# Performance work log

Measured on AMD Instinct MI355X. Metric: run time of the kernel, lower is better.

Reference implementation:

```python
import jax, jax.numpy as jnp
import numpy as np

B, D_IN, NQ, H = 65536, 385, 64, 16  # batch, input dim, num questions, head width
DIMS = [385, 512, 256, 192]


def setup_inputs() -> dict:
    key = jax.random.key(0)
    ks = jax.random.split(key, 12)
    s = 0.02
    inp = {
        "x": jax.random.normal(ks[0], (B, D_IN), jnp.float32),
        "W1": jax.random.normal(ks[1], (DIMS[0], DIMS[1]), jnp.float32) * s,
        "b1": jnp.zeros((DIMS[1],), jnp.float32),
        "W2": jax.random.normal(ks[2], (DIMS[1], DIMS[2]), jnp.float32) * s,
        "b2": jnp.zeros((DIMS[2],), jnp.float32),
        "W3": jax.random.normal(ks[3], (DIMS[2], DIMS[3]), jnp.float32) * s,
        "b3": jnp.zeros((DIMS[3],), jnp.float32),
        # all true/false heads stacked: layout [qid, correct, H] flattened on last axis
        "Wh": jax.random.normal(ks[4], (DIMS[3], NQ * 2 * H), jnp.float32) * s,
        "bh": jnp.zeros((NQ * 2 * H,), jnp.float32),
        "question_ids": jax.random.randint(ks[5], (B,), 0, NQ, jnp.int32),
        "is_correct": jax.random.randint(ks[6], (B,), 0, 2, jnp.int32),
    }
    return inp


def reference(x, W1, b1, W2, b2, W3, b3, Wh, bh, question_ids, is_correct):
    # shared trunk (dropout is identity at eval); activation = relu
    h = jax.nn.relu(x @ W1 + b1)          # [B, 512]
    h = jax.nn.relu(h @ W2 + b2)          # [B, 256]
    h = jax.nn.relu(h @ W3 + b3)          # [B, 192] shared features
    # compute all heads densely, then gather the per-row head slice —
    # equivalent to routing each row to its (question_id, is_correct) Linear head
    logits_all = h @ Wh + bh              # [B, NQ*2*H]
    base = (question_ids * 2 + is_correct) * H        # [B]
    idx = base[:, None] + jnp.arange(H)[None, :]      # [B, H]
    return jnp.take_along_axis(logits_all, idx, axis=1)  # [B, H]
```

## Files before the change

### kernel.cpp

```cpp
#include <hip/hip_runtime.h>
#include <hip/hip_bf16.h>

#define THREADS 1024
#define ROWS 64

typedef __attribute__((ext_vector_type(4))) float f32x4;
typedef __attribute__((ext_vector_type(8))) short s16x8;

__device__ __forceinline__ unsigned short bfbits(float f) {
  __bf16 h = (__bf16)f;
  return __builtin_bit_cast(unsigned short, h);
}
__device__ __forceinline__ float bf2f(unsigned short h) {
  unsigned u = ((unsigned)h) << 16;
  return __builtin_bit_cast(float, u);
}

__global__ void prep_kernel(const float* __restrict__ W1, const float* __restrict__ W2,
                            const float* __restrict__ W3, const float* __restrict__ Wh,
                            unsigned short* __restrict__ w1f, unsigned short* __restrict__ w2f,
                            unsigned short* __restrict__ w3f, unsigned short* __restrict__ whT) {
  int u = blockIdx.x * blockDim.x + threadIdx.x;
  const int U1 = 24576, U2 = 16384, U3 = 6144, U4 = 49152;
  if (u < U1) {
    int lane = u & 63, r = (u >> 6) & 31, c = u >> 11;
    int f  = r * 16 + (lane & 15);
    int kb = c * 32 + ((lane >> 4) << 3);
    s16x8 v;
    #pragma unroll
    for (int j = 0; j < 8; ++j) v[j] = (short)bfbits(W1[(kb + j) * 512 + f]);
    *(s16x8*)(w1f + (u << 3)) = v;
    return;
  }
  u -= U1;
  if (u < U2) {
    int lane = u & 63, r = (u >> 6) & 15, c = u >> 10;
    int f  = r * 16 + (lane & 15);
    int kb = c * 32 + ((lane >> 4) << 3);
    s16x8 v;
    #pragma unroll
    for (int j = 0; j < 8; ++j) v[j] = (short)bfbits(W2[(kb + j) * 256 + f]);
    *(s16x8*)(w2f + (u << 3)) = v;
    return;
  }
  u -= U2;
  if (u < U3) {
    int lane = u & 63, t = u >> 6;
    int c = t / 12, r = t - c * 12;
    int f  = r * 16 + (lane & 15);
    int kb = c * 32 + ((lane >> 4) << 3);
    s16x8 v;
    #pragma unroll
    for (int j = 0; j < 8; ++j) v[j] = (short)bfbits(W3[(kb + j) * 192 + f]);
    *(s16x8*)(w3f + (u << 3)) = v;
    return;
  }
  u -= U3;
  if (u < U4) {
    int j = u & 15, v2 = u >> 4;
    int fo = v2 % 24, head = v2 / 24;
    s16x8 v;
    #pragma unroll
    for (int i = 0; i < 8; ++i) v[i] = (short)bfbits(Wh[(fo * 8 + i) * 2048 + head * 16 + j]);
    *(s16x8*)(whT + u * 8) = v;
  }
}

#define MFMA(a, b, c) __builtin_amdgcn_mfma_f32_16x16x32_bf16((a), (b), (c), 0, 0, 0)
#define SWZ(lane) (((lane) * 16) ^ ((((lane) >> 4) & 3) << 5))

__global__ __launch_bounds__(THREADS, 4)
void fused_mlp(const float* __restrict__ x,
               const float* __restrict__ b1,
               const float* __restrict__ b2,
               const float* __restrict__ b3,
               const float* __restrict__ bh,
               const float* __restrict__ W1,
               const int* __restrict__ qid,
               const int* __restrict__ corr,
               const unsigned short* __restrict__ w1f,
               const unsigned short* __restrict__ w2f,
               const unsigned short* __restrict__ w3f,
               const unsigned short* __restrict__ whT,
               float* __restrict__ out) {
  __shared__ __align__(16) unsigned char lds[120832];
  unsigned char* xall = lds;
  unsigned char* h1f  = lds + 49152;
  unsigned char* h2f  = lds;
  float* h3p          = (float*)(lds + 49152);
  float* b1s  = (float*)(lds + 114688);
  float* b2s  = (float*)(lds + 116736);
  float* b3s  = (float*)(lds + 117760);
  float* w1l  = (float*)(lds + 118528);
  float* x384 = (float*)(lds + 120576);

  const int tid  = threadIdx.x;
  const int lane = tid & 63;
  const int w    = tid >> 6;
  const int b0   = blockIdx.x * ROWS;
  const int l15  = lane & 15;
  const int lh   = lane >> 4;

  const int s_kh = tid & 3;
  const int s_sr = (tid >> 2) & 63;
  const int s_cl = tid >> 8;
  const int s_off = ((s_sr >> 4) << 10) + SWZ((s_sr & 15) + (s_kh << 4));
  const float* s_x = x + (size_t)(b0 + s_sr) * 385 + (s_kh << 3);

  f32x4 lo, hi;
  auto sload = [&](int p) {
    int c = (p << 2) + s_cl;
    lo = *(const f32x4*)(s_x + c * 32);
    hi = *(const f32x4*)(s_x + c * 32 + 4);
  };
  auto swrite = [&](int p) {
    int c = (p << 2) + s_cl;
    s16x8 v;
    v[0] = (short)bfbits(lo[0]); v[1] = (short)bfbits(lo[1]);
    v[2] = (short)bfbits(lo[2]); v[3] = (short)bfbits(lo[3]);
    v[4] = (short)bfbits(hi[0]); v[5] = (short)bfbits(hi[1]);
    v[6] = (short)bfbits(hi[2]); v[7] = (short)bfbits(hi[3]);
    *(s16x8*)(xall + (c << 12) + s_off) = v;
  };

  sload(0);
  if (tid < 512)                    { b1s[tid] = b1[tid]; w1l[tid] = W1[384 * 512 + tid]; }
  else if (tid < 768)               { b2s[tid - 512] = b2[tid - 512]; }
  else if (tid < 960)               { b3s[tid - 768] = b3[tid - 768]; }
  else                              { x384[tid - 960] = x[(size_t)(b0 + tid - 960) * 385 + 384]; }
  swrite(0);
  __syncthreads();

  f32x4 acc1[2][4];
  #pragma unroll
  for (int a = 0; a < 2; ++a)
    #pragma unroll
    for (int bt = 0; bt < 4; ++bt) acc1[a][bt] = (f32x4)0.0f;

  const int swz_l = SWZ(lane);

#define G1_CHUNKS(C0, C1)                                                              \
  _Pragma("unroll")                                                                    \
  for (int c = C0; c < C1; ++c) {                                                      \
    s16x8 a0 = *(const s16x8*)(w1f + (((c * 32 + w * 2 + 0) * 64 + lane) << 3));       \
    s16x8 a1 = *(const s16x8*)(w1f + (((c * 32 + w * 2 + 1) * 64 + lane) << 3));       \
    _Pragma("unroll")                                                                  \
    for (int bt = 0; bt < 4; ++bt) {                                                   \
      s16x8 bfr = *(const s16x8*)(xall + (c << 12) + (bt << 10) + swz_l);              \
      acc1[0][bt] = MFMA(a0, bfr, acc1[0][bt]);                                        \
      acc1[1][bt] = MFMA(a1, bfr, acc1[1][bt]);                                        \
    }                                                                                  \
  }

  sload(1);
  G1_CHUNKS(0, 4)
  swrite(1);
  __syncthreads();

  sload(2);
  G1_CHUNKS(4, 8)
  swrite(2);
  __syncthreads();

  G1_CHUNKS(8, 12)

  #pragma unroll
  for (int a = 0; a < 2; ++a) {
    int ft = w * 2 + a;
    int fb = (ft << 4) + (lh << 2);
    f32x4 bv = *(const f32x4*)(b1s + fb);
    f32x4 wv = *(const f32x4*)(w1l + fb);
    int kh = ((a << 1) + (lh >> 1)) & 3;
    int so = SWZ(l15 + (kh << 4)) + ((lh & 1) << 3);
    #pragma unroll
    for (int bt = 0; bt < 4; ++bt) {
      float xv = x384[(bt << 4) + l15];
      float v0 = fmaxf(acc1[a][bt][0] + bv[0] + wv[0] * xv, 0.f);
      float v1 = fmaxf(acc1[a][bt][1] + bv[1] + wv[1] * xv, 0.f);
      float v2 = fmaxf(acc1[a][bt][2] + bv[2] + wv[2] * xv, 0.f);
      float v3 = fmaxf(acc1[a][bt][3] + bv[3] + wv[3] * xv, 0.f);
      unsigned plo = (unsigned)bfbits(v0) | ((unsigned)bfbits(v1) << 16);
      unsigned phi = (unsigned)bfbits(v2) | ((unsigned)bfbits(v3) << 16);
      unsigned long long pk = (unsigned long long)plo | ((unsigned long long)phi << 32);
      *(unsigned long long*)(h1f + (((w << 2) + bt) << 10) + so) = pk;
    }
  }
  __syncthreads();

  f32x4 acc2[4];
  #pragma unroll
  for (int bt = 0; bt < 4; ++bt) acc2[bt] = (f32x4)0.0f;

  #pragma unroll
  for (int c = 0; c < 16; ++c) {
    s16x8 a2 = *(const s16x8*)(w2f + (((c * 16 + w) * 64 + lane) << 3));
    #pragma unroll
    for (int bt = 0; bt < 4; ++bt) {
      s16x8 bfr = *(const s16x8*)(h1f + ((c << 12) + (bt << 10)) + swz_l);
      acc2[bt] = MFMA(a2, bfr, acc2[bt]);
    }
  }

  {
    int fb = (w << 4) + (lh << 2);
    f32x4 bv = *(const f32x4*)(b2s + fb);
    int kh = (((w & 1) << 1) + (lh >> 1)) & 3;
    int so = SWZ(l15 + (kh << 4)) + ((lh & 1) << 3);
    #pragma unroll
    for (int bt = 0; bt < 4; ++bt) {
      float v0 = fmaxf(acc2[bt][0] + bv[0], 0.f);
      float v1 = fmaxf(acc2[bt][1] + bv[1], 0.f);
      float v2 = fmaxf(acc2[bt][2] + bv[2], 0.f);
      float v3 = fmaxf(acc2[bt][3] + bv[3], 0.f);
      unsigned plo = (unsigned)bfbits(v0) | ((unsigned)bfbits(v1) << 16);
      unsigned phi = (unsigned)bfbits(v2) | ((unsigned)bfbits(v3) << 16);
      unsigned long long pk = (unsigned long long)plo | ((unsigned long long)phi << 32);
      *(unsigned long long*)(h2f + ((((w >> 1) << 2) + bt) << 10) + so) = pk;
    }
  }
  __syncthreads();

  if (w < 12) {
    f32x4 acc3[4];
    #pragma unroll
    for (int bt = 0; bt < 4; ++bt) acc3[bt] = (f32x4)0.0f;

    #pragma unroll
    for (int c = 0; c < 8; ++c) {
      s16x8 a3 = *(const s16x8*)(w3f + (((c * 12 + w) * 64 + lane) << 3));
      #pragma unroll
      for (int bt = 0; bt < 4; ++bt) {
        s16x8 bfr = *(const s16x8*)(h2f + ((c << 12) + (bt << 10)) + swz_l);
        acc3[bt] = MFMA(a3, bfr, acc3[bt]);
      }
    }

    int fb = (w << 4) + (lh << 2);
    f32x4 bv = *(const f32x4*)(b3s + fb);
    #pragma unroll
    for (int bt = 0; bt < 4; ++bt) {
      int bb = (bt << 4) + l15;
      f32x4 vv;
      vv[0] = fmaxf(acc3[bt][0] + bv[0], 0.f);
      vv[1] = fmaxf(acc3[bt][1] + bv[1], 0.f);
      vv[2] = fmaxf(acc3[bt][2] + bv[2], 0.f);
      vv[3] = fmaxf(acc3[bt][3] + bv[3], 0.f);
      *(f32x4*)(h3p + bb * 204 + fb) = vv;
    }
  }
  __syncthreads();

  {
    int bb = tid >> 4, j = tid & 15;
    int gb = b0 + bb;
    int head = qid[gb] * 2 + corr[gb];
    const unsigned short* wp = whT + ((head * 24) * 16 + j) * 8;
    const float* hp = h3p + bb * 204;
    float acc = bh[(head << 4) + j];
    #pragma unroll 6
    for (int fo = 0; fo < 24; ++fo) {
      s16x8 wv = *(const s16x8*)(wp + fo * 128);
      f32x4 h0 = *(const f32x4*)(hp + fo * 8);
      f32x4 h1v = *(const f32x4*)(hp + fo * 8 + 4);
      acc += bf2f((unsigned short)wv[0]) * h0[0] + bf2f((unsigned short)wv[1]) * h0[1]
           + bf2f((unsigned short)wv[2]) * h0[2] + bf2f((unsigned short)wv[3]) * h0[3]
           + bf2f((unsigned short)wv[4]) * h1v[0] + bf2f((unsigned short)wv[5]) * h1v[1]
           + bf2f((unsigned short)wv[6]) * h1v[2] + bf2f((unsigned short)wv[7]) * h1v[3];
    }
    out[(size_t)gb * 16 + j] = acc;
  }
}

extern "C" void kernel_launch(void* const* d_in, const int* in_sizes, int n_in,
                              void* d_out, int out_size, void* d_ws, size_t ws_size,
                              hipStream_t stream) {
  (void)in_sizes; (void)n_in; (void)out_size; (void)ws_size;
  const float* x  = (const float*)d_in[0];
  const float* W1 = (const float*)d_in[1];
  const float* b1 = (const float*)d_in[2];
  const float* W2 = (const float*)d_in[3];
  const float* b2 = (const float*)d_in[4];
  const float* W3 = (const float*)d_in[5];
  const float* b3 = (const float*)d_in[6];
  const float* Wh = (const float*)d_in[7];
  const float* bh = (const float*)d_in[8];
  const int* qid  = (const int*)d_in[9];
  const int* corr = (const int*)d_in[10];
  float* out = (float*)d_out;

  unsigned short* w1f = (unsigned short*)d_ws;
  unsigned short* w2f = w1f + 12 * 32 * 64 * 8;
  unsigned short* w3f = w2f + 16 * 16 * 64 * 8;
  unsigned short* whT = w3f + 8 * 12 * 64 * 8;

  prep_kernel<<<376, 256, 0, stream>>>(W1, W2, W3, Wh, w1f, w2f, w3f, whT);
  fused_mlp<<<65536 / ROWS, THREADS, 0, stream>>>(x, b1, b2, b3, bh, W1, qid, corr,
                                                  w1f, w2f, w3f, whT, out);
}
```

Baseline: 85.03 us.

## Double rows per block and split layer-1 features into two halves interleaved with layer 2

Each block now handles 128 rows instead of 64, so each weight fragment loaded from global is reused across twice as many rows. Layer 1 is computed in two 256-feature halves, each immediately consumed by half of the layer-2 K loop, so the 512-wide h1 never has to sit in LDS all at once. Biases are read straight from global instead of being staged in LDS, and h3 is kept as bf16 rather than fp32 to fit the 160KB LDS buffer. The cost is higher LDS use and register pressure, which may limit occupancy, half as many blocks, and extra rounding of h3 to bf16.

```diff
diff --git a/kernel.cpp b/kernel.cpp
--- a/kernel.cpp
+++ b/kernel.cpp
@@ -2,7 +2,7 @@
 #include <hip/hip_bf16.h>
 
 #define THREADS 1024
-#define ROWS 64
+#define ROWS 128
 
 typedef __attribute__((ext_vector_type(4))) float f32x4;
 typedef __attribute__((ext_vector_type(8))) short s16x8;
@@ -67,7 +67,18 @@
 }
 
 #define MFMA(a, b, c) __builtin_amdgcn_mfma_f32_16x16x32_bf16((a), (b), (c), 0, 0, 0)
-#define SWZ(lane) (((lane) * 16) ^ ((((lane) >> 4) & 3) << 5))
+#define SWZ(lp) (((lp) * 16) ^ ((((lp) >> 4) & 3) << 5))
+
+#define G1_RANGE(P, C0, C1)                                                          \
+  _Pragma("unroll")                                                                  \
+  for (int c = (C0); c < (C1); ++c) {                                                \
+    s16x8 af = *(const s16x8*)(w1f + (((c * 32 + (P) * 16 + w) * 64 + lane) << 3));  \
+    _Pragma("unroll")                                                                \
+    for (int bt = 0; bt < 8; ++bt) {                                                 \
+      s16x8 bfr = *(const s16x8*)(xall + (c << 13) + (bt << 10) + swz_l);            \
+      acc1[bt] = MFMA(af, bfr, acc1[bt]);                                            \
+    }                                                                                \
+  }
 
 __global__ __launch_bounds__(THREADS, 4)
 void fused_mlp(const float* __restrict__ x,
@@ -83,16 +94,11 @@
                const unsigned short* __restrict__ w3f,
                const unsigned short* __restrict__ whT,
                float* __restrict__ out) {
-  __shared__ __align__(16) unsigned char lds[120832];
-  unsigned char* xall = lds;
-  unsigned char* h1f  = lds + 49152;
-  unsigned char* h2f  = lds;
-  float* h3p          = (float*)(lds + 49152);
-  float* b1s  = (float*)(lds + 114688);
-  float* b2s  = (float*)(lds + 116736);
-  float* b3s  = (float*)(lds + 117760);
-  float* w1l  = (float*)(lds + 118528);
-  float* x384 = (float*)(lds + 120576);
+  __shared__ __align__(16) unsigned char lds[163840];
+  unsigned char*  xall = lds;
+  unsigned char*  h1f  = lds + 98304;
+  unsigned char*  h2f  = lds;
+  unsigned short* h3b  = (unsigned short*)(lds + 98304);
 
   const int tid  = threadIdx.x;
   const int lane = tid & 63;
@@ -100,114 +106,113 @@
   const int b0   = blockIdx.x * ROWS;
   const int l15  = lane & 15;
   const int lh   = lane >> 4;
-
-  const int s_kh = tid & 3;
-  const int s_sr = (tid >> 2) & 63;
-  const int s_cl = tid >> 8;
-  const int s_off = ((s_sr >> 4) << 10) + SWZ((s_sr & 15) + (s_kh << 4));
-  const float* s_x = x + (size_t)(b0 + s_sr) * 385 + (s_kh << 3);
-
-  f32x4 lo, hi;
-  auto sload = [&](int p) {
-    int c = (p << 2) + s_cl;
-    lo = *(const f32x4*)(s_x + c * 32);
-    hi = *(const f32x4*)(s_x + c * 32 + 4);
+  const int swz_l = SWZ(lane);
+
+  const int hrow = tid >> 4, hj = tid & 15;
+  const int head0 = qid[b0 + hrow] * 2 + corr[b0 + hrow];
+  const int head1 = qid[b0 + 64 + hrow] * 2 + corr[b0 + 64 + hrow];
+  float xv384[8];
+  #pragma unroll
+  for (int bt = 0; bt < 8; ++bt)
+    xv384[bt] = x[(size_t)(b0 + bt * 16 + l15) * 385 + 384];
+
+  f32x4 sv[2][2];
+  int s_ad[2];
+  auto sload = [&](int g) {
+    #pragma unroll
+    for (int q = 0; q < 2; ++q) {
+      int fi = q * 1024 + tid;
+      int c  = (g << 2) + (fi >> 9);
+      int wi = fi & 511;
+      int bt = wi >> 6, lp = wi & 63;
+      int row = (bt << 4) + (lp & 15);
+      int k   = c * 32 + ((lp >> 4) << 3);
+      const float* p = x + (size_t)(b0 + row) * 385 + k;
+      sv[q][0] = *(const f32x4*)p;
+      sv[q][1] = *(const f32x4*)(p + 4);
+      s_ad[q] = (c << 13) + (bt << 10) + SWZ(lp);
+    }
   };
-  auto swrite = [&](int p) {
-    int c = (p << 2) + s_cl;
-    s16x8 v;
-    v[0] = (short)bfbits(lo[0]); v[1] = (short)bfbits(lo[1]);
-    v[2] = (short)bfbits(lo[2]); v[3] = (short)bfbits(lo[3]);
-    v[4] = (short)bfbits(hi[0]); v[5] = (short)bfbits(hi[1]);
-    v[6] = (short)bfbits(hi[2]); v[7] = (short)bfbits(hi[3]);
-    *(s16x8*)(xall + (c << 12) + s_off) = v;
+  auto swrite = [&]() {
+    #pragma unroll
+    for (int q = 0; q < 2; ++q) {
+      s16x8 v;
+      v[0] = (short)bfbits(sv[q][0][0]); v[1] = (short)bfbits(sv[q][0][1]);
+      v[2] = (short)bfbits(sv[q][0][2]); v[3] = (short)bfbits(sv[q][0][3]);
+      v[4] = (short)bfbits(sv[q][1][0]); v[5] = (short)bfbits(sv[q][1][1]);
+      v[6] = (short)bfbits(sv[q][1][2]); v[7] = (short)bfbits(sv[q][1][3]);
+      *(s16x8*)(xall + s_ad[q]) = v;
+    }
   };
 
-  sload(0);
-  if (tid < 512)                    { b1s[tid] = b1[tid]; w1l[tid] = W1[384 * 512 + tid]; }
-  else if (tid < 768)               { b2s[tid - 512] = b2[tid - 512]; }
-  else if (tid < 960)               { b3s[tid - 768] = b3[tid - 768]; }
-  else                              { x384[tid - 960] = x[(size_t)(b0 + tid - 960) * 385 + 384]; }
-  swrite(0);
-  __syncthreads();
-
-  f32x4 acc1[2][4];
+  f32x4 acc1[8], acc2[8];
   #pragma unroll
-  for (int a = 0; a < 2; ++a)
-    #pragma unroll
-    for (int bt = 0; bt < 4; ++bt) acc1[a][bt] = (f32x4)0.0f;
-
-  const int swz_l = SWZ(lane);
-
-#define G1_CHUNKS(C0, C1)                                                              \
-  _Pragma("unroll")                                                                    \
-  for (int c = C0; c < C1; ++c) {                                                      \
-    s16x8 a0 = *(const s16x8*)(w1f + (((c * 32 + w * 2 + 0) * 64 + lane) << 3));       \
-    s16x8 a1 = *(const s16x8*)(w1f + (((c * 32 + w * 2 + 1) * 64 + lane) << 3));       \
-    _Pragma("unroll")                                                                  \
-    for (int bt = 0; bt < 4; ++bt) {                                                   \
-      s16x8 bfr = *(const s16x8*)(xall + (c << 12) + (bt << 10) + swz_l);              \
-      acc1[0][bt] = MFMA(a0, bfr, acc1[0][bt]);                                        \
-      acc1[1][bt] = MFMA(a1, bfr, acc1[1][bt]);                                        \
-    }                                                                                  \
-  }
-
-  sload(1);
-  G1_CHUNKS(0, 4)
-  swrite(1);
-  __syncthreads();
-
-  sload(2);
-  G1_CHUNKS(4, 8)
-  swrite(2);
-  __syncthreads();
-
-  G1_CHUNKS(8, 12)
-
-  #pragma unroll
-  for (int a = 0; a < 2; ++a) {
-    int ft = w * 2 + a;
-    int fb = (ft << 4) + (lh << 2);
-    f32x4 bv = *(const f32x4*)(b1s + fb);
-    f32x4 wv = *(const f32x4*)(w1l + fb);
-    int kh = ((a << 1) + (lh >> 1)) & 3;
-    int so = SWZ(l15 + (kh << 4)) + ((lh & 1) << 3);
-    #pragma unroll
-    for (int bt = 0; bt < 4; ++bt) {
-      float xv = x384[(bt << 4) + l15];
-      float v0 = fmaxf(acc1[a][bt][0] + bv[0] + wv[0] * xv, 0.f);
-      float v1 = fmaxf(acc1[a][bt][1] + bv[1] + wv[1] * xv, 0.f);
-      float v2 = fmaxf(acc1[a][bt][2] + bv[2] + wv[2] * xv, 0.f);
-      float v3 = fmaxf(acc1[a][bt][3] + bv[3] + wv[3] * xv, 0.f);
+  for (int bt = 0; bt < 8; ++bt) { acc1[bt] = (f32x4)0.0f; acc2[bt] = (f32x4)0.0f; }
+
+  auto epi1 = [&](int P) {
+    int fg = P * 256 + w * 16 + lh * 4;
+    f32x4 bv = *(const f32x4*)(b1 + fg);
+    f32x4 wv = *(const f32x4*)(W1 + 384 * 512 + fg);
+    int so = ((w >> 1) << 13) + SWZ(l15 + (((2 * w + (lh >> 1)) & 3) << 4)) + ((lh & 1) << 3);
+    #pragma unroll
+    for (int bt = 0; bt < 8; ++bt) {
+      float xv = xv384[bt];
+      float v0 = fmaxf(acc1[bt][0] + bv[0] + wv[0] * xv, 0.f);
+      float v1 = fmaxf(acc1[bt][1] + bv[1] + wv[1] * xv, 0.f);
+      float v2 = fmaxf(acc1[bt][2] + bv[2] + wv[2] * xv, 0.f);
+      float v3 = fmaxf(acc1[bt][3] + bv[3] + wv[3] * xv, 0.f);
       unsigned plo = (unsigned)bfbits(v0) | ((unsigned)bfbits(v1) << 16);
       unsigned phi = (unsigned)bfbits(v2) | ((unsigned)bfbits(v3) << 16);
       unsigned long long pk = (unsigned long long)plo | ((unsigned long long)phi << 32);
-      *(unsigned long long*)(h1f + (((w << 2) + bt) << 10) + so) = pk;
-    }
-  }
-  __syncthreads();
-
-  f32x4 acc2[4];
-  #pragma unroll
-  for (int bt = 0; bt < 4; ++bt) acc2[bt] = (f32x4)0.0f;
-
-  #pragma unroll
-  for (int c = 0; c < 16; ++c) {
-    s16x8 a2 = *(const s16x8*)(w2f + (((c * 16 + w) * 64 + lane) << 3));
-    #pragma unroll
-    for (int bt = 0; bt < 4; ++bt) {
-      s16x8 bfr = *(const s16x8*)(h1f + ((c << 12) + (bt << 10)) + swz_l);
-      acc2[bt] = MFMA(a2, bfr, acc2[bt]);
-    }
-  }
-
+      *(unsigned long long*)(h1f + so + (bt << 10)) = pk;
+      acc1[bt] = (f32x4)0.0f;
+    }
+  };
+
+  auto g2half = [&](int c0) {
+    #pragma unroll
+    for (int ci = 0; ci < 8; ++ci) {
+      int c = c0 + ci;
+      s16x8 a2 = *(const s16x8*)(w2f + (((c * 16 + w) * 64 + lane) << 3));
+      #pragma unroll
+      for (int bt = 0; bt < 8; ++bt) {
+        s16x8 bfr = *(const s16x8*)(h1f + (ci << 13) + (bt << 10) + swz_l);
+        acc2[bt] = MFMA(a2, bfr, acc2[bt]);
+      }
+    }
+  };
+
+  sload(0); swrite();
+  __syncthreads();
+
+  sload(1);
+  G1_RANGE(0, 0, 4)
+  swrite();
+  __syncthreads();
+
+  sload(2);
+  G1_RANGE(0, 4, 8)
+  swrite();
+  __syncthreads();
+
+  G1_RANGE(0, 8, 12)
+  epi1(0);
+  __syncthreads();
+
+  g2half(0);
+  __syncthreads();
+
+  G1_RANGE(1, 0, 12)
+  epi1(1);
+  __syncthreads();
+
+  g2half(8);
   {
-    int fb = (w << 4) + (lh << 2);
-    f32x4 bv = *(const f32x4*)(b2s + fb);
-    int kh = (((w & 1) << 1) + (lh >> 1)) & 3;
-    int so = SWZ(l15 + (kh << 4)) + ((lh & 1) << 3);
-    #pragma unroll
-    for (int bt = 0; bt < 4; ++bt) {
+    int fg = w * 16 + lh * 4;
+    f32x4 bv = *(const f32x4*)(b2 + fg);
+    int so = ((w >> 1) << 13) + SWZ(l15 + (((2 * w + (lh >> 1)) & 3) << 4)) + ((lh & 1) << 3);
+    #pragma unroll
+    for (int bt = 0; bt < 8; ++bt) {
       float v0 = fmaxf(acc2[bt][0] + bv[0], 0.f);
       float v1 = fmaxf(acc2[bt][1] + bv[1], 0.f);
       float v2 = fmaxf(acc2[bt][2] + bv[2], 0.f);
@@ -215,59 +220,57 @@
       unsigned plo = (unsigned)bfbits(v0) | ((unsigned)bfbits(v1) << 16);
       unsigned phi = (unsigned)bfbits(v2) | ((unsigned)bfbits(v3) << 16);
       unsigned long long pk = (unsigned long long)plo | ((unsigned long long)phi << 32);
-      *(unsigned long long*)(h2f + ((((w >> 1) << 2) + bt) << 10) + so) = pk;
+      *(unsigned long long*)(h2f + so + (bt << 10)) = pk;
     }
   }
   __syncthreads();
 
   if (w < 12) {
-    f32x4 acc3[4];
-    #pragma unroll
-    for (int bt = 0; bt < 4; ++bt) acc3[bt] = (f32x4)0.0f;
-
+    f32x4 acc3[8];
+    #pragma unroll
+    for (int bt = 0; bt < 8; ++bt) acc3[bt] = (f32x4)0.0f;
     #pragma unroll
     for (int c = 0; c < 8; ++c) {
       s16x8 a3 = *(const s16x8*)(w3f + (((c * 12 + w) * 64 + lane) << 3));
       #pragma unroll
-      for (int bt = 0; bt < 4; ++bt) {
-        s16x8 bfr = *(const s16x8*)(h2f + ((c << 12) + (bt << 10)) + swz_l);
+      for (int bt = 0; bt < 8; ++bt) {
+        s16x8 bfr = *(const s16x8*)(h2f + (c << 13) + (bt << 10) + swz_l);
         acc3[bt] = MFMA(a3, bfr, acc3[bt]);
       }
     }
-
-    int fb = (w << 4) + (lh << 2);
-    f32x4 bv = *(const f32x4*)(b3s + fb);
-    #pragma unroll
-    for (int bt = 0; bt < 4; ++bt) {
-      int bb = (bt << 4) + l15;
-      f32x4 vv;
-      vv[0] = fmaxf(acc3[bt][0] + bv[0], 0.f);
-      vv[1] = fmaxf(acc3[bt][1] + bv[1], 0.f);
-      vv[2] = fmaxf(acc3[bt][2] + bv[2], 0.f);
-      vv[3] = fmaxf(acc3[bt][3] + bv[3], 0.f);
-      *(f32x4*)(h3p + bb * 204 + fb) = vv;
-    }
-  }
-  __syncthreads();
-
-  {
-    int bb = tid >> 4, j = tid & 15;
-    int gb = b0 + bb;
-    int head = qid[gb] * 2 + corr[gb];
-    const unsigned short* wp = whT + ((head * 24) * 16 + j) * 8;
-    const float* hp = h3p + bb * 204;
-    float acc = bh[(head << 4) + j];
+    int fg = w * 16 + lh * 4;
+    f32x4 bv = *(const f32x4*)(b3 + fg);
+    #pragma unroll
+    for (int bt = 0; bt < 8; ++bt) {
+      int row = (bt << 4) + l15;
+      float v0 = fmaxf(acc3[bt][0] + bv[0], 0.f);
+      float v1 = fmaxf(acc3[bt][1] + bv[1], 0.f);
+      float v2 = fmaxf(acc3[bt][2] + bv[2], 0.f);
+      float v3 = fmaxf(acc3[bt][3] + bv[3], 0.f);
+      unsigned plo = (unsigned)bfbits(v0) | ((unsigned)bfbits(v1) << 16);
+      unsigned phi = (unsigned)bfbits(v2) | ((unsigned)bfbits(v3) << 16);
+      unsigned long long pk = (unsigned long long)plo | ((unsigned long long)phi << 32);
+      *(unsigned long long*)((unsigned char*)h3b + row * 400 + w * 32 + lh * 8) = pk;
+    }
+  }
+  __syncthreads();
+
+  #pragma unroll
+  for (int q = 0; q < 2; ++q) {
+    int row  = q * 64 + hrow;
+    int head = q ? head1 : head0;
+    const unsigned short* wp = whT + ((head * 24) * 16 + hj) * 8;
+    const unsigned short* hp = h3b + row * 200;
+    float acc = bh[(head << 4) + hj];
     #pragma unroll 6
     for (int fo = 0; fo < 24; ++fo) {
       s16x8 wv = *(const s16x8*)(wp + fo * 128);
-      f32x4 h0 = *(const f32x4*)(hp + fo * 8);
-      f32x4 h1v = *(const f32x4*)(hp + fo * 8 + 4);
-      acc += bf2f((unsigned short)wv[0]) * h0[0] + bf2f((unsigned short)wv[1]) * h0[1]
-           + bf2f((unsigned short)wv[2]) * h0[2] + bf2f((unsigned short)wv[3]) * h0[3]
-           + bf2f((unsigned short)wv[4]) * h1v[0] + bf2f((unsigned short)wv[5]) * h1v[1]
-           + bf2f((unsigned short)wv[6]) * h1v[2] + bf2f((unsigned short)wv[7]) * h1v[3];
-    }
-    out[(size_t)gb * 16 + j] = acc;
+      s16x8 hv = *(const s16x8*)(hp + fo * 8);
+      #pragma unroll
+      for (int e = 0; e < 8; ++e)
+        acc += bf2f((unsigned short)wv[e]) * bf2f((unsigned short)hv[e]);
+    }
+    out[(size_t)(b0 + row) * 16 + hj] = acc;
   }
 }
 
```

Result: slower. 139.2 us (+63.8%).
